# Kernel tuning notes

Measured on AMD Instinct MI355X. Metric: run time of the kernel, lower is better.

The kernel has to match this reference:

```python
import jax, jax.numpy as jnp
import numpy as np

N_NODES = 100000
N_EDGES = 1600000
IN_CH = 128
HID = 128
OUT_CH = 10


def setup_inputs() -> dict:
    key = jax.random.key(0)
    ks = jax.random.split(key, 14)
    s_in = 1.0 / np.sqrt(IN_CH)
    s_h = 1.0 / np.sqrt(HID)
    return {
        "x0": jax.random.normal(ks[0], (N_NODES, IN_CH), jnp.float32),
        "edge_index": jax.random.randint(ks[1], (2, N_EDGES), 0, N_NODES, jnp.int32),
        "edge_weight": jax.random.uniform(ks[2], (N_EDGES,), jnp.float32),
        # GraphConv layer 1 (in -> hid): lin_rel (weight+bias) applied to aggregated msgs, lin_root (no bias)
        "W1_rel": jax.random.uniform(ks[3], (IN_CH, HID), jnp.float32, -s_in, s_in),
        "b1": jax.random.uniform(ks[4], (HID,), jnp.float32, -s_in, s_in),
        "W1_root": jax.random.uniform(ks[5], (IN_CH, HID), jnp.float32, -s_in, s_in),
        # GraphConv layer 2 (hid -> hid)
        "W2_rel": jax.random.uniform(ks[6], (HID, HID), jnp.float32, -s_h, s_h),
        "b2": jax.random.uniform(ks[7], (HID,), jnp.float32, -s_h, s_h),
        "W2_root": jax.random.uniform(ks[8], (HID, HID), jnp.float32, -s_h, s_h),
        # GraphConv layer 3 (hid -> hid)
        "W3_rel": jax.random.uniform(ks[9], (HID, HID), jnp.float32, -s_h, s_h),
        "b3": jax.random.uniform(ks[10], (HID,), jnp.float32, -s_h, s_h),
        "W3_root": jax.random.uniform(ks[11], (HID, HID), jnp.float32, -s_h, s_h),
        # classification head
        "W_lin": jax.random.uniform(ks[12], (HID, OUT_CH), jnp.float32, -s_h, s_h),
        "b_lin": jax.random.uniform(ks[13], (OUT_CH,), jnp.float32, -s_h, s_h),
    }


def _graph_conv(x, src, dst, ew, W_rel, b_rel, W_root):
    # message: x_j * w_e ; aggregate: scatter-add onto dst ; update: lin_rel(agg) + lin_root(x)
    msg = x[src] * ew[:, None]                                   # [E, C]
    agg = jax.ops.segment_sum(msg, dst, num_segments=x.shape[0])  # [N, C]
    return agg @ W_rel + b_rel + x @ W_root                      # [N, C']


def reference(x0, edge_index, edge_weight,
              W1_rel, b1, W1_root,
              W2_rel, b2, W2_root,
              W3_rel, b3, W3_root,
              W_lin, b_lin):
    src, dst = edge_index[0], edge_index[1]
    # dropout p=0.2 is identity in eval mode
    x1 = jax.nn.relu(_graph_conv(x0, src, dst, edge_weight, W1_rel, b1, W1_root))
    x2 = jax.nn.relu(_graph_conv(x1, src, dst, edge_weight, W2_rel, b2, W2_root))
    x3 = jax.nn.relu(_graph_conv(x2, src, dst, edge_weight, W3_rel, b3, W3_root))
    logits = x3 @ W_lin + b_lin
    return jax.nn.log_softmax(logits, axis=-1)
```

## Files before the change

### kernel.cpp

```cpp
#include <hip/hip_runtime.h>
#include <hip/hip_bf16.h>
#include <math.h>

#define C128 128
#define OUT_CH 10

typedef __attribute__((ext_vector_type(8))) short short8;
typedef __attribute__((ext_vector_type(4))) float f32x4;
typedef __attribute__((ext_vector_type(2))) float f32x2;
typedef __attribute__((ext_vector_type(4))) int i32x4;

__device__ __forceinline__ unsigned short f2bf(float f) {
    unsigned b = __float_as_uint(f);
    unsigned r = (b + 0x7FFF + ((b >> 16) & 1)) >> 16;
    return (unsigned short)r;
}
__device__ __forceinline__ float bf2f(unsigned short u) {
    return __uint_as_float(((unsigned)u) << 16);
}


#define NBMAX 400
#define BCAP  4608
#define P1K   4096

__global__ __launch_bounds__(512) void bin_kernel(
    const int* __restrict__ ei, const float* __restrict__ ew,
    int* __restrict__ gcur, unsigned* __restrict__ bins_rec,
    unsigned char* __restrict__ bins_dst, int E, int nb)
{
    __shared__ int cnt[NBMAX];
    __shared__ int pos[NBMAX];
    __shared__ int gbase[NBMAX];
    __shared__ int s[512];
    __shared__ int totalSh;
    __shared__ uint2 buf[P1K];

    const int t = threadIdx.x;
    const int e0 = blockIdx.x * P1K;

    for (int b = t; b < nb; b += 512) { cnt[b] = 0; pos[b] = 0; }
    __syncthreads();

    unsigned rec[8];
    int dstv[8];
    const int e = e0 + t * 8;
    if (e + 8 <= E) {
        i32x4 d0 = __builtin_nontemporal_load((const i32x4*)(ei + E + e));
        i32x4 d1 = __builtin_nontemporal_load((const i32x4*)(ei + E + e + 4));
        i32x4 s0 = __builtin_nontemporal_load((const i32x4*)(ei + e));
        i32x4 s1 = __builtin_nontemporal_load((const i32x4*)(ei + e + 4));
        f32x4 w0 = __builtin_nontemporal_load((const f32x4*)(ew + e));
        f32x4 w1 = __builtin_nontemporal_load((const f32x4*)(ew + e + 4));
        int dd[8] = {d0.x, d0.y, d0.z, d0.w, d1.x, d1.y, d1.z, d1.w};
        int ss[8] = {s0.x, s0.y, s0.z, s0.w, s1.x, s1.y, s1.z, s1.w};
        float ww[8] = {w0.x, w0.y, w0.z, w0.w, w1.x, w1.y, w1.z, w1.w};
#pragma unroll
        for (int j = 0; j < 8; ++j) {
            unsigned wb = __float_as_uint(ww[j]);
            unsigned r  = ((wb + 0x7FFF + ((wb >> 16) & 1)) >> 16) & 0x7FFFu;
            rec[j]  = (unsigned)ss[j] | (r << 17);
            dstv[j] = dd[j];
            atomicAdd(&cnt[dd[j] >> 8], 1);
        }
    } else {
#pragma unroll
        for (int j = 0; j < 8; ++j) {
            int ee = e + j;
            if (ee < E) {
                int dst = ei[E + ee];
                unsigned wb = __float_as_uint(ew[ee]);
                unsigned r  = ((wb + 0x7FFF + ((wb >> 16) & 1)) >> 16) & 0x7FFFu;
                rec[j]  = (unsigned)ei[ee] | (r << 17);
                dstv[j] = dst;
                atomicAdd(&cnt[dst >> 8], 1);
            } else {
                dstv[j] = -1;
            }
        }
    }
    __syncthreads();

    int c = (t < nb) ? cnt[t] : 0;
    s[t] = c;
    __syncthreads();
    for (int o = 1; o < 512; o <<= 1) {
        int u = (t >= o) ? s[t - o] : 0;
        __syncthreads();
        s[t] += u;
        __syncthreads();
    }
    if (t == nb - 1) totalSh = s[t];
    __syncthreads();

#pragma unroll
    for (int j = 0; j < 8; ++j) {
        if (dstv[j] >= 0) {
            int b = dstv[j] >> 8;
            int r = atomicAdd(&pos[b], 1);
            buf[s[b] - cnt[b] + r] = make_uint2(rec[j], (unsigned)dstv[j]);
        }
    }
    __syncthreads();

    if (t < nb) {
        int b = t + (int)((blockIdx.x * 131u) % (unsigned)nb);
        if (b >= nb) b -= nb;
        int cb = cnt[b];
        if (cb > 0) gbase[b] = atomicAdd(&gcur[b], cb);
    }
    __syncthreads();

    const int total = totalSh;
    for (int i = t; i < total; i += 512) {
        uint2 v = buf[i];
        int b = (int)(v.y >> 8);
        int dest = gbase[b] + (i - (s[b] - cnt[b]));
        if (dest < BCAP) {
            bins_rec[(size_t)b * BCAP + dest] = v.x;
            bins_dst[(size_t)b * BCAP + dest] = (unsigned char)(v.y & 255u);
        }
    }
}

__global__ __launch_bounds__(512) void bucket_scan_kernel(
    const int* __restrict__ gcur, int* __restrict__ bbase,
    int* __restrict__ row_ptr, int nb, int N, int E)
{
    __shared__ int s[512];
    int t = threadIdx.x;
    int v = (t < nb) ? gcur[t] : 0;
    s[t] = v;
    __syncthreads();
    for (int o = 1; o < 512; o <<= 1) {
        int u = (t >= o) ? s[t - o] : 0;
        __syncthreads();
        s[t] += u;
        __syncthreads();
    }
    if (t < nb) bbase[t] = s[t] - v;
    if (t == 0) row_ptr[N] = E;
}

__global__ __launch_bounds__(256) void build_kernel(
    const unsigned* __restrict__ bins_rec, const unsigned char* __restrict__ bins_dst,
    const int* __restrict__ gcur, const int* __restrict__ bbase,
    int* __restrict__ row_ptr, unsigned* __restrict__ csr, int N)
{
    __shared__ int rowCnt[256];
    __shared__ int rowOff[256];
    __shared__ int sc[256];
    __shared__ unsigned out[BCAP];

    const int b = blockIdx.x, t = threadIdx.x;
    int cnt = gcur[b];
    if (cnt > BCAP) cnt = BCAP;
    const int base = bbase[b];
    const unsigned* mbr = bins_rec + (size_t)b * BCAP;
    const unsigned char* mbd = bins_dst + (size_t)b * BCAP;

    rowCnt[t] = 0;
    __syncthreads();
    for (int i = t; i < cnt; i += 256) atomicAdd(&rowCnt[(int)mbd[i]], 1);
    __syncthreads();

    int v = rowCnt[t];
    sc[t] = v;
    __syncthreads();
    for (int o = 1; o < 256; o <<= 1) {
        int u = (t >= o) ? sc[t - o] : 0;
        __syncthreads();
        sc[t] += u;
        __syncthreads();
    }
    rowOff[t] = sc[t] - v;
    int idx = b * 256 + t;
    if (idx <= N) row_ptr[idx] = base + sc[t] - v;
    rowCnt[t] = 0;
    __syncthreads();

    for (int i = t; i < cnt; i += 256) {
        int d = (int)mbd[i];
        int k = atomicAdd(&rowCnt[d], 1);
        out[rowOff[d] + k] = mbr[i];
    }
    __syncthreads();

    for (int i = t; i < cnt; i += 256) csr[base + i] = out[i];
}


__global__ __launch_bounds__(256) void cvt_both_kernel(const float4* __restrict__ x,
                                                       ushort4* __restrict__ xb,
                                                       unsigned* __restrict__ xf8, int n4) {
    int i = blockIdx.x * blockDim.x + threadIdx.x;
    if (i < n4) {
        float4 v = x[i];
        ushort4 o;
        o.x = f2bf(v.x); o.y = f2bf(v.y); o.z = f2bf(v.z); o.w = f2bf(v.w);
        xb[i] = o;
        unsigned p = __builtin_amdgcn_cvt_pk_fp8_f32(v.x, v.y, 0, false);
        p = __builtin_amdgcn_cvt_pk_fp8_f32(v.z, v.w, p, true);
        xf8[i] = p;
    }
}


__global__ __launch_bounds__(256) void pack_all_kernel(
    const float* __restrict__ W1r, const float* __restrict__ W1t,
    const float* __restrict__ W2r, const float* __restrict__ W2t,
    const float* __restrict__ W3r, const float* __restrict__ W3t,
    const float* __restrict__ Wl,
    unsigned short* __restrict__ Wp1, unsigned short* __restrict__ Wp2,
    unsigned short* __restrict__ Wp3, unsigned short* __restrict__ WlP)
{
    int b = blockIdx.x;
    if (b < 384) {
        int which = b >> 7;
        const float* Wr = (which == 0) ? W1r : (which == 1) ? W2r : W3r;
        const float* Wt = (which == 0) ? W1t : (which == 1) ? W2t : W3t;
        unsigned short* Wp = (which == 0) ? Wp1 : (which == 1) ? Wp2 : Wp3;
        int idx = (b & 127) * 256 + threadIdx.x;
        int j    = idx & 7;
        int n    = (idx >> 3) & 127;
        int quad = (idx >> 10) & 3;
        int ks   = idx >> 12;
        const float* W = (ks < 4) ? Wr : Wt;
        int k = (ks & 3) * 32 + quad * 8 + j;
        Wp[idx] = f2bf(W[(size_t)k * C128 + n]);
    } else {
        int idx = (b - 384) * 256 + threadIdx.x;
        int j    = idx & 7;
        int col  = (idx >> 3) & 15;
        int quad = (idx >> 7) & 3;
        int ks   = (idx >> 9) & 3;
        int half = idx >> 11;
        int k = ks * 32 + quad * 8 + j;
        float v = (col < OUT_CH) ? Wl[(size_t)k * OUT_CH + col] : 0.f;
        unsigned short hi = f2bf(v);
        unsigned short outv = hi;
        if (half) outv = f2bf(v - bf2f(hi));
        WlP[idx] = outv;
    }
}


__global__ __launch_bounds__(256) void gather_fp8_kernel(
    const unsigned* __restrict__ xf8,
    const int* __restrict__ row_ptr,
    const unsigned* __restrict__ csr, unsigned short* __restrict__ aggb, int N)
{
    int node = blockIdx.x * 4 + (threadIdx.x >> 6);
    if (node >= N) return;
    int lane = threadIdx.x & 63;
    int g   = lane >> 4;
    int l16 = lane & 15;
    int i0  = row_ptr[node];
    int deg = row_ptr[node + 1] - i0;

    f32x2 acc2[4];
#pragma unroll
    for (int j = 0; j < 4; ++j) acc2[j] = (f32x2){0.f, 0.f};

    for (int base = 0; base < deg; base += 64) {
        int rem = deg - base; if (rem > 64) rem = 64;
        int rec = 0;
        if (base + lane < deg)
            rec = (int)__builtin_nontemporal_load(&csr[i0 + base + lane]);

        for (int c = 0; c < rem; c += 16) {
            int i0e = c + g, i1e = c + 4 + g, i2e = c + 8 + g, i3e = c + 12 + g;
            int s0 = __shfl(rec, i0e & 63, 64);
            int s1 = __shfl(rec, i1e & 63, 64);
            int s2 = __shfl(rec, i2e & 63, 64);
            int s3 = __shfl(rec, i3e & 63, 64);
            float w0 = (i0e < rem) ? __uint_as_float(((unsigned)s0 >> 17) << 16) : 0.f;
            float w1 = (i1e < rem) ? __uint_as_float(((unsigned)s1 >> 17) << 16) : 0.f;
            float w2 = (i2e < rem) ? __uint_as_float(((unsigned)s2 >> 17) << 16) : 0.f;
            float w3 = (i3e < rem) ? __uint_as_float(((unsigned)s3 >> 17) << 16) : 0.f;
            uint2 q0 = *(const uint2*)&xf8[(unsigned)(s0 & 0x1FFFF) * 32u + l16 * 2];
            uint2 q1 = *(const uint2*)&xf8[(unsigned)(s1 & 0x1FFFF) * 32u + l16 * 2];
            uint2 q2 = *(const uint2*)&xf8[(unsigned)(s2 & 0x1FFFF) * 32u + l16 * 2];
            uint2 q3 = *(const uint2*)&xf8[(unsigned)(s3 & 0x1FFFF) * 32u + l16 * 2];
#define ACCUM(q, wv)                                                         \
            {                                                                \
                f32x2 w2v = {(wv), (wv)};                                    \
                acc2[0] += __builtin_amdgcn_cvt_pk_f32_fp8((q).x, false) * w2v; \
                acc2[1] += __builtin_amdgcn_cvt_pk_f32_fp8((q).x, true)  * w2v; \
                acc2[2] += __builtin_amdgcn_cvt_pk_f32_fp8((q).y, false) * w2v; \
                acc2[3] += __builtin_amdgcn_cvt_pk_f32_fp8((q).y, true)  * w2v; \
            }
            ACCUM(q0, w0) ACCUM(q1, w1) ACCUM(q2, w2) ACCUM(q3, w3)
#undef ACCUM
        }
    }

#pragma unroll
    for (int j = 0; j < 4; ++j) {
        acc2[j].x += __shfl_xor(acc2[j].x, 16, 64);
        acc2[j].y += __shfl_xor(acc2[j].y, 16, 64);
        acc2[j].x += __shfl_xor(acc2[j].x, 32, 64);
        acc2[j].y += __shfl_xor(acc2[j].y, 32, 64);
    }
    if (g == 0) {
        uint4 o;
        o.x = (unsigned)f2bf(acc2[0].x) | ((unsigned)f2bf(acc2[0].y) << 16);
        o.y = (unsigned)f2bf(acc2[1].x) | ((unsigned)f2bf(acc2[1].y) << 16);
        o.z = (unsigned)f2bf(acc2[2].x) | ((unsigned)f2bf(acc2[2].y) << 16);
        o.w = (unsigned)f2bf(acc2[3].x) | ((unsigned)f2bf(acc2[3].y) << 16);
        *(uint4*)&aggb[(size_t)node * C128 + l16 * 8] = o;
    }
}


__global__ __launch_bounds__(256) void gemm_slim(
    const unsigned short* __restrict__ aggb, const unsigned short* __restrict__ xb,
    const unsigned short* __restrict__ Wp, const float* __restrict__ bias,
    unsigned short* __restrict__ outb, unsigned char* __restrict__ outf8, int N)
{
    const int t = threadIdx.x;
    const int w    = t >> 6;
    const int lane = t & 63;
    const int l15  = lane & 15;
    const int quad = lane >> 4;
    const int wnode0 = blockIdx.x * 64 + w * 16;

    int arow = wnode0 + l15;
    if (arow >= N) arow = N - 1;

    short8 a[8];
#pragma unroll
    for (int k = 0; k < 4; ++k)
        a[k] = *(const short8*)&aggb[(size_t)arow * C128 + k * 32 + quad * 8];
#pragma unroll
    for (int k = 0; k < 4; ++k)
        a[4 + k] = *(const short8*)&xb[(size_t)arow * C128 + k * 32 + quad * 8];

    float bv[8];
#pragma unroll
    for (int nt = 0; nt < 8; ++nt) bv[nt] = bias[nt * 16 + l15];

    f32x4 acc[8];
#pragma unroll
    for (int nt = 0; nt < 8; ++nt) acc[nt] = (f32x4){0.f, 0.f, 0.f, 0.f};

#pragma unroll
    for (int ks = 0; ks < 8; ++ks) {
#pragma unroll
        for (int nt = 0; nt < 8; ++nt) {
            short8 b = *(const short8*)&Wp[(((ks * 4 + quad) * 128) + nt * 16 + l15) * 8];
            acc[nt] = __builtin_amdgcn_mfma_f32_16x16x32_bf16(a[ks], b, acc[nt], 0, 0, 0);
        }
    }

#pragma unroll
    for (int r = 0; r < 4; ++r) {
        int row = wnode0 + quad * 4 + r;
        if (row < N) {
#pragma unroll
            for (int nt = 0; nt < 8; ++nt) {
                float v = fmaxf(acc[nt][r] + bv[nt], 0.f);
                outb[(size_t)row * C128 + nt * 16 + l15] = f2bf(v);
                unsigned p8 = __builtin_amdgcn_cvt_pk_fp8_f32(v, 0.f, 0, false);
                outf8[(size_t)row * C128 + nt * 16 + l15] = (unsigned char)(p8 & 0xff);
            }
        }
    }
}


__global__ __launch_bounds__(256) void gemm_head(
    const unsigned short* __restrict__ aggb, const unsigned short* __restrict__ xb,
    const unsigned short* __restrict__ Wp, const float* __restrict__ bias,
    const unsigned short* __restrict__ WlP, const float* __restrict__ bl,
    float* __restrict__ out, int N)
{
    __shared__ unsigned short X3[4][16 * C128];

    const int t = threadIdx.x;
    const int w    = t >> 6;
    const int lane = t & 63;
    const int l15  = lane & 15;
    const int quad = lane >> 4;
    const int wnode0 = blockIdx.x * 64 + w * 16;

    int arow = wnode0 + l15;
    if (arow >= N) arow = N - 1;

    short8 a[8];
#pragma unroll
    for (int k = 0; k < 4; ++k)
        a[k] = *(const short8*)&aggb[(size_t)arow * C128 + k * 32 + quad * 8];
#pragma unroll
    for (int k = 0; k < 4; ++k)
        a[4 + k] = *(const short8*)&xb[(size_t)arow * C128 + k * 32 + quad * 8];

    float bv[8];
#pragma unroll
    for (int nt = 0; nt < 8; ++nt) bv[nt] = bias[nt * 16 + l15];

    f32x4 acc[8];
#pragma unroll
    for (int nt = 0; nt < 8; ++nt) acc[nt] = (f32x4){0.f, 0.f, 0.f, 0.f};

#pragma unroll
    for (int ks = 0; ks < 8; ++ks) {
#pragma unroll
        for (int nt = 0; nt < 8; ++nt) {
            short8 b = *(const short8*)&Wp[(((ks * 4 + quad) * 128) + nt * 16 + l15) * 8];
            acc[nt] = __builtin_amdgcn_mfma_f32_16x16x32_bf16(a[ks], b, acc[nt], 0, 0, 0);
        }
    }

#pragma unroll
    for (int r = 0; r < 4; ++r) {
        int lrow = quad * 4 + r;
#pragma unroll
        for (int nt = 0; nt < 8; ++nt) {
            float v = fmaxf(acc[nt][r] + bv[nt], 0.f);
            X3[w][lrow * C128 + nt * 16 + l15] = f2bf(v);
        }
    }

    f32x4 hacc = (f32x4){0.f, 0.f, 0.f, 0.f};
#pragma unroll
    for (int ks = 0; ks < 4; ++ks) {
        short8 a2 = *(const short8*)&X3[w][l15 * C128 + ks * 32 + quad * 8];
        short8 bh = *(const short8*)&WlP[(((ks * 4 + quad) * 16) + l15) * 8];
        short8 bl2 = *(const short8*)&WlP[2048 + (((ks * 4 + quad) * 16) + l15) * 8];
        hacc = __builtin_amdgcn_mfma_f32_16x16x32_bf16(a2, bh, hacc, 0, 0, 0);
        hacc = __builtin_amdgcn_mfma_f32_16x16x32_bf16(a2, bl2, hacc, 0, 0, 0);
    }

    float blv = (l15 < OUT_CH) ? bl[l15] : 0.f;
#pragma unroll
    for (int r = 0; r < 4; ++r) {
        int row = wnode0 + quad * 4 + r;
        float lg = (l15 < OUT_CH) ? (hacc[r] + blv) : -1e30f;
        float m = lg;
        m = fmaxf(m, __shfl_xor(m, 1, 64));
        m = fmaxf(m, __shfl_xor(m, 2, 64));
        m = fmaxf(m, __shfl_xor(m, 4, 64));
        m = fmaxf(m, __shfl_xor(m, 8, 64));
        float s = __expf(lg - m);
        s += __shfl_xor(s, 1, 64);
        s += __shfl_xor(s, 2, 64);
        s += __shfl_xor(s, 4, 64);
        s += __shfl_xor(s, 8, 64);
        float lse = m + __logf(s);
        if (l15 < OUT_CH && row < N)
            out[(size_t)row * OUT_CH + l15] = lg - lse;
    }
}


extern "C" void kernel_launch(void* const* d_in, const int* in_sizes, int n_in,
                              void* d_out, int out_size, void* d_ws, size_t ws_size,
                              hipStream_t stream) {
    const float* x0   = (const float*)d_in[0];
    const int*   ei   = (const int*)  d_in[1];
    const float* ew   = (const float*)d_in[2];
    const float* W1r  = (const float*)d_in[3];
    const float* b1   = (const float*)d_in[4];
    const float* W1t  = (const float*)d_in[5];
    const float* W2r  = (const float*)d_in[6];
    const float* b2   = (const float*)d_in[7];
    const float* W2t  = (const float*)d_in[8];
    const float* W3r  = (const float*)d_in[9];
    const float* b3   = (const float*)d_in[10];
    const float* W3t  = (const float*)d_in[11];
    const float* Wlin = (const float*)d_in[12];
    const float* blin = (const float*)d_in[13];

    const int N = in_sizes[0] / C128;
    const int E = in_sizes[1] / 2;
    const int nb = (N + 255) >> 8;

    char* ws = (char*)d_ws;
    size_t off = 0;
    auto alloc = [&](size_t bytes) {
        void* p = ws + off;
        off = (off + bytes + 255) & ~(size_t)255;
        return p;
    };
    size_t bb = (size_t)N * C128 * sizeof(unsigned short);
    size_t fb = (size_t)N * C128;
    unsigned short* aggb = (unsigned short*)alloc(bb);
    unsigned short* xb0  = (unsigned short*)alloc(bb);
    unsigned short* xb1  = (unsigned short*)alloc(bb);
    unsigned char*  xf8  = (unsigned char*)alloc(fb);
    unsigned short* Wp1  = (unsigned short*)alloc(32768 * 2);
    unsigned short* Wp2  = (unsigned short*)alloc(32768 * 2);
    unsigned short* Wp3  = (unsigned short*)alloc(32768 * 2);
    unsigned short* WlP  = (unsigned short*)alloc(4096 * 2);
    unsigned* csr  = (unsigned*)alloc((size_t)E * 4);
    int* row_ptr   = (int*)alloc((size_t)(N + 2) * 4);
    unsigned* bins_rec  = (unsigned*)alloc((size_t)nb * BCAP * 4);
    unsigned char* bins_dst = (unsigned char*)alloc((size_t)nb * BCAP);
    int* gcur      = (int*)alloc((size_t)nb * 4);
    int* bbase     = (int*)alloc((size_t)nb * 4);

    hipMemsetAsync(gcur, 0, (size_t)nb * sizeof(int), stream);
    bin_kernel<<<(E + P1K - 1) / P1K, 512, 0, stream>>>(ei, ew, gcur, bins_rec, bins_dst, E, nb);
    bucket_scan_kernel<<<1, 512, 0, stream>>>(gcur, bbase, row_ptr, nb, N, E);
    build_kernel<<<nb, 256, 0, stream>>>(bins_rec, bins_dst, gcur, bbase, row_ptr, csr, N);

    cvt_both_kernel<<<(N * C128 / 4 + 255) / 256, 256, 0, stream>>>(
        (const float4*)x0, (ushort4*)xb0, (unsigned*)xf8, N * C128 / 4);
    pack_all_kernel<<<400, 256, 0, stream>>>(W1r, W1t, W2r, W2t, W3r, W3t, Wlin,
                                             Wp1, Wp2, Wp3, WlP);

    int gatherGrid = (N + 3) / 4;
    int gemmGrid   = (N + 63) / 64;

    gather_fp8_kernel<<<gatherGrid, 256, 0, stream>>>(
        (const unsigned*)xf8, row_ptr, csr, aggb, N);
    gemm_slim<<<gemmGrid, 256, 0, stream>>>(aggb, xb0, Wp1, b1, xb1, xf8, N);
    gather_fp8_kernel<<<gatherGrid, 256, 0, stream>>>(
        (const unsigned*)xf8, row_ptr, csr, aggb, N);
    gemm_slim<<<gemmGrid, 256, 0, stream>>>(aggb, xb1, Wp2, b2, xb0, xf8, N);
    gather_fp8_kernel<<<gatherGrid, 256, 0, stream>>>(
        (const unsigned*)xf8, row_ptr, csr, aggb, N);
    gemm_head<<<gemmGrid, 256, 0, stream>>>(aggb, xb0, Wp3, b3, WlP, blin,
                                            (float*)d_out, N);
}
```

Measured before the change: 374.7 us.

## Fuse neighbor gather with per-layer GEMM via shared-memory tiles

```diff
diff --git a/kernel.cpp b/kernel.cpp
--- a/kernel.cpp
+++ b/kernel.cpp
@@ -245,211 +245,274 @@
 }
 
 
-__global__ __launch_bounds__(256) void gather_fp8_kernel(
+#define AGS 136
+
+__global__ __launch_bounds__(256) void fused_layer(
     const unsigned* __restrict__ xf8,
     const int* __restrict__ row_ptr,
-    const unsigned* __restrict__ csr, unsigned short* __restrict__ aggb, int N)
-{
-    int node = blockIdx.x * 4 + (threadIdx.x >> 6);
-    if (node >= N) return;
-    int lane = threadIdx.x & 63;
-    int g   = lane >> 4;
-    int l16 = lane & 15;
-    int i0  = row_ptr[node];
-    int deg = row_ptr[node + 1] - i0;
-
-    f32x2 acc2[4];
-#pragma unroll
-    for (int j = 0; j < 4; ++j) acc2[j] = (f32x2){0.f, 0.f};
-
-    for (int base = 0; base < deg; base += 64) {
-        int rem = deg - base; if (rem > 64) rem = 64;
-        int rec = 0;
-        if (base + lane < deg)
-            rec = (int)__builtin_nontemporal_load(&csr[i0 + base + lane]);
-
-        for (int c = 0; c < rem; c += 16) {
-            int i0e = c + g, i1e = c + 4 + g, i2e = c + 8 + g, i3e = c + 12 + g;
-            int s0 = __shfl(rec, i0e & 63, 64);
-            int s1 = __shfl(rec, i1e & 63, 64);
-            int s2 = __shfl(rec, i2e & 63, 64);
-            int s3 = __shfl(rec, i3e & 63, 64);
-            float w0 = (i0e < rem) ? __uint_as_float(((unsigned)s0 >> 17) << 16) : 0.f;
-            float w1 = (i1e < rem) ? __uint_as_float(((unsigned)s1 >> 17) << 16) : 0.f;
-            float w2 = (i2e < rem) ? __uint_as_float(((unsigned)s2 >> 17) << 16) : 0.f;
-            float w3 = (i3e < rem) ? __uint_as_float(((unsigned)s3 >> 17) << 16) : 0.f;
-            uint2 q0 = *(const uint2*)&xf8[(unsigned)(s0 & 0x1FFFF) * 32u + l16 * 2];
-            uint2 q1 = *(const uint2*)&xf8[(unsigned)(s1 & 0x1FFFF) * 32u + l16 * 2];
-            uint2 q2 = *(const uint2*)&xf8[(unsigned)(s2 & 0x1FFFF) * 32u + l16 * 2];
-            uint2 q3 = *(const uint2*)&xf8[(unsigned)(s3 & 0x1FFFF) * 32u + l16 * 2];
-#define ACCUM(q, wv)                                                         \
-            {                                                                \
-                f32x2 w2v = {(wv), (wv)};                                    \
-                acc2[0] += __builtin_amdgcn_cvt_pk_f32_fp8((q).x, false) * w2v; \
-                acc2[1] += __builtin_amdgcn_cvt_pk_f32_fp8((q).x, true)  * w2v; \
-                acc2[2] += __builtin_amdgcn_cvt_pk_f32_fp8((q).y, false) * w2v; \
-                acc2[3] += __builtin_amdgcn_cvt_pk_f32_fp8((q).y, true)  * w2v; \
-            }
-            ACCUM(q0, w0) ACCUM(q1, w1) ACCUM(q2, w2) ACCUM(q3, w3)
-#undef ACCUM
-        }
-    }
-
-#pragma unroll
-    for (int j = 0; j < 4; ++j) {
-        acc2[j].x += __shfl_xor(acc2[j].x, 16, 64);
-        acc2[j].y += __shfl_xor(acc2[j].y, 16, 64);
-        acc2[j].x += __shfl_xor(acc2[j].x, 32, 64);
-        acc2[j].y += __shfl_xor(acc2[j].y, 32, 64);
-    }
-    if (g == 0) {
-        uint4 o;
-        o.x = (unsigned)f2bf(acc2[0].x) | ((unsigned)f2bf(acc2[0].y) << 16);
-        o.y = (unsigned)f2bf(acc2[1].x) | ((unsigned)f2bf(acc2[1].y) << 16);
-        o.z = (unsigned)f2bf(acc2[2].x) | ((unsigned)f2bf(acc2[2].y) << 16);
-        o.w = (unsigned)f2bf(acc2[3].x) | ((unsigned)f2bf(acc2[3].y) << 16);
-        *(uint4*)&aggb[(size_t)node * C128 + l16 * 8] = o;
-    }
-}
-
-
-__global__ __launch_bounds__(256) void gemm_slim(
-    const unsigned short* __restrict__ aggb, const unsigned short* __restrict__ xb,
-    const unsigned short* __restrict__ Wp, const float* __restrict__ bias,
+    const unsigned* __restrict__ csr,
+    const unsigned short* __restrict__ xb,
+    const unsigned short* __restrict__ Wp,
+    const float* __restrict__ bias,
     unsigned short* __restrict__ outb, unsigned char* __restrict__ outf8, int N)
 {
+    __shared__ unsigned short AG[16 * AGS];
+    __shared__ unsigned short XR[16 * AGS];
+
     const int t = threadIdx.x;
     const int w    = t >> 6;
     const int lane = t & 63;
-    const int l15  = lane & 15;
-    const int quad = lane >> 4;
-    const int wnode0 = blockIdx.x * 64 + w * 16;
-
-    int arow = wnode0 + l15;
-    if (arow >= N) arow = N - 1;
-
-    short8 a[8];
-#pragma unroll
-    for (int k = 0; k < 4; ++k)
-        a[k] = *(const short8*)&aggb[(size_t)arow * C128 + k * 32 + quad * 8];
-#pragma unroll
-    for (int k = 0; k < 4; ++k)
-        a[4 + k] = *(const short8*)&xb[(size_t)arow * C128 + k * 32 + quad * 8];
-
-    float bv[8];
-#pragma unroll
-    for (int nt = 0; nt < 8; ++nt) bv[nt] = bias[nt * 16 + l15];
-
-    f32x4 acc[8];
-#pragma unroll
-    for (int nt = 0; nt < 8; ++nt) acc[nt] = (f32x4){0.f, 0.f, 0.f, 0.f};
+    const int l16  = lane & 15;
+    const int g    = lane >> 4;
+    const int tile0 = blockIdx.x * 16;
+
+    {
+        int rrow = tile0 + w * 4 + g;
+        int srow = (rrow < N) ? rrow : 0;
+        uint4 v = *(const uint4*)&xb[(size_t)srow * C128 + l16 * 8];
+        *(uint4*)&XR[(w * 4 + g) * AGS + l16 * 8] = v;
+    }
+
+    for (int i = 0; i < 4; ++i) {
+        int node = tile0 + w * 4 + i;
+        int i0 = 0, deg = 0;
+        if (node < N) { i0 = row_ptr[node]; deg = row_ptr[node + 1] - i0; }
+
+        f32x2 acc2[4];
+#pragma unroll
+        for (int j = 0; j < 4; ++j) acc2[j] = (f32x2){0.f, 0.f};
+
+        for (int base = 0; base < deg; base += 64) {
+            int rem = deg - base; if (rem > 64) rem = 64;
+            int rec = 0;
+            if (base + lane < deg)
+                rec = (int)__builtin_nontemporal_load(&csr[i0 + base + lane]);
+
+            for (int c = 0; c < rem; c += 16) {
+                int i0e = c + g, i1e = c + 4 + g, i2e = c + 8 + g, i3e = c + 12 + g;
+                int s0 = __shfl(rec, i0e & 63, 64);
+                int s1 = __shfl(rec, i1e & 63, 64);
+                int s2 = __shfl(rec, i2e & 63, 64);
+                int s3 = __shfl(rec, i3e & 63, 64);
+                float w0 = (i0e < rem) ? __uint_as_float(((unsigned)s0 >> 17) << 16) : 0.f;
+                float w1 = (i1e < rem) ? __uint_as_float(((unsigned)s1 >> 17) << 16) : 0.f;
+                float w2 = (i2e < rem) ? __uint_as_float(((unsigned)s2 >> 17) << 16) : 0.f;
+                float w3 = (i3e < rem) ? __uint_as_float(((unsigned)s3 >> 17) << 16) : 0.f;
+                uint2 q0 = *(const uint2*)&xf8[(unsigned)(s0 & 0x1FFFF) * 32u + l16 * 2];
+                uint2 q1 = *(const uint2*)&xf8[(unsigned)(s1 & 0x1FFFF) * 32u + l16 * 2];
+                uint2 q2 = *(const uint2*)&xf8[(unsigned)(s2 & 0x1FFFF) * 32u + l16 * 2];
+                uint2 q3 = *(const uint2*)&xf8[(unsigned)(s3 & 0x1FFFF) * 32u + l16 * 2];
+#define ACCUM(q, wv)                                                         \
+                {                                                            \
+                    f32x2 w2v = {(wv), (wv)};                                \
+                    acc2[0] += __builtin_amdgcn_cvt_pk_f32_fp8((q).x, false) * w2v; \
+                    acc2[1] += __builtin_amdgcn_cvt_pk_f32_fp8((q).x, true)  * w2v; \
+                    acc2[2] += __builtin_amdgcn_cvt_pk_f32_fp8((q).y, false) * w2v; \
+                    acc2[3] += __builtin_amdgcn_cvt_pk_f32_fp8((q).y, true)  * w2v; \
+                }
+                ACCUM(q0, w0) ACCUM(q1, w1) ACCUM(q2, w2) ACCUM(q3, w3)
+#undef ACCUM
+            }
+        }
+
+#pragma unroll
+        for (int j = 0; j < 4; ++j) {
+            acc2[j].x += __shfl_xor(acc2[j].x, 16, 64);
+            acc2[j].y += __shfl_xor(acc2[j].y, 16, 64);
+            acc2[j].x += __shfl_xor(acc2[j].x, 32, 64);
+            acc2[j].y += __shfl_xor(acc2[j].y, 32, 64);
+        }
+        if (g == 0) {
+            uint4 o;
+            o.x = (unsigned)f2bf(acc2[0].x) | ((unsigned)f2bf(acc2[0].y) << 16);
+            o.y = (unsigned)f2bf(acc2[1].x) | ((unsigned)f2bf(acc2[1].y) << 16);
+            o.z = (unsigned)f2bf(acc2[2].x) | ((unsigned)f2bf(acc2[2].y) << 16);
+            o.w = (unsigned)f2bf(acc2[3].x) | ((unsigned)f2bf(acc2[3].y) << 16);
+            *(uint4*)&AG[(w * 4 + i) * AGS + l16 * 8] = o;
+        }
+    }
+    __syncthreads();
+
+    const int l15 = l16, quad = g;
+    const int nt0 = 2 * w, nt1 = 2 * w + 1;
+    float bv0 = bias[nt0 * 16 + l15];
+    float bv1 = bias[nt1 * 16 + l15];
+    f32x4 acc0 = (f32x4){0.f, 0.f, 0.f, 0.f};
+    f32x4 acc1 = (f32x4){0.f, 0.f, 0.f, 0.f};
 
 #pragma unroll
     for (int ks = 0; ks < 8; ++ks) {
-#pragma unroll
-        for (int nt = 0; nt < 8; ++nt) {
-            short8 b = *(const short8*)&Wp[(((ks * 4 + quad) * 128) + nt * 16 + l15) * 8];
-            acc[nt] = __builtin_amdgcn_mfma_f32_16x16x32_bf16(a[ks], b, acc[nt], 0, 0, 0);
-        }
+        short8 a;
+        if (ks < 4) a = *(const short8*)&AG[l15 * AGS + ks * 32 + quad * 8];
+        else        a = *(const short8*)&XR[l15 * AGS + (ks - 4) * 32 + quad * 8];
+        short8 b0 = *(const short8*)&Wp[(((ks * 4 + quad) * 128) + nt0 * 16 + l15) * 8];
+        short8 b1 = *(const short8*)&Wp[(((ks * 4 + quad) * 128) + nt1 * 16 + l15) * 8];
+        acc0 = __builtin_amdgcn_mfma_f32_16x16x32_bf16(a, b0, acc0, 0, 0, 0);
+        acc1 = __builtin_amdgcn_mfma_f32_16x16x32_bf16(a, b1, acc1, 0, 0, 0);
     }
 
 #pragma unroll
     for (int r = 0; r < 4; ++r) {
-        int row = wnode0 + quad * 4 + r;
+        int row = tile0 + quad * 4 + r;
         if (row < N) {
-#pragma unroll
-            for (int nt = 0; nt < 8; ++nt) {
-                float v = fmaxf(acc[nt][r] + bv[nt], 0.f);
-                outb[(size_t)row * C128 + nt * 16 + l15] = f2bf(v);
-                unsigned p8 = __builtin_amdgcn_cvt_pk_fp8_f32(v, 0.f, 0, false);
-                outf8[(size_t)row * C128 + nt * 16 + l15] = (unsigned char)(p8 & 0xff);
-            }
-        }
-    }
-}
-
-
-__global__ __launch_bounds__(256) void gemm_head(
-    const unsigned short* __restrict__ aggb, const unsigned short* __restrict__ xb,
-    const unsigned short* __restrict__ Wp, const float* __restrict__ bias,
+            float v0 = fmaxf(acc0[r] + bv0, 0.f);
+            float v1 = fmaxf(acc1[r] + bv1, 0.f);
+            outb[(size_t)row * C128 + nt0 * 16 + l15] = f2bf(v0);
+            outb[(size_t)row * C128 + nt1 * 16 + l15] = f2bf(v1);
+            unsigned p0 = __builtin_amdgcn_cvt_pk_fp8_f32(v0, 0.f, 0, false);
+            unsigned p1 = __builtin_amdgcn_cvt_pk_fp8_f32(v1, 0.f, 0, false);
+            outf8[(size_t)row * C128 + nt0 * 16 + l15] = (unsigned char)(p0 & 0xff);
+            outf8[(size_t)row * C128 + nt1 * 16 + l15] = (unsigned char)(p1 & 0xff);
+        }
+    }
+}
+
+
+__global__ __launch_bounds__(256) void fused_layer_head(
+    const unsigned* __restrict__ xf8,
+    const int* __restrict__ row_ptr,
+    const unsigned* __restrict__ csr,
+    const unsigned short* __restrict__ xb,
+    const unsigned short* __restrict__ Wp,
+    const float* __restrict__ bias,
     const unsigned short* __restrict__ WlP, const float* __restrict__ bl,
     float* __restrict__ out, int N)
 {
-    __shared__ unsigned short X3[4][16 * C128];
+    __shared__ unsigned short AG[16 * AGS];
+    __shared__ unsigned short XR[16 * AGS];
 
     const int t = threadIdx.x;
     const int w    = t >> 6;
     const int lane = t & 63;
-    const int l15  = lane & 15;
-    const int quad = lane >> 4;
-    const int wnode0 = blockIdx.x * 64 + w * 16;
-
-    int arow = wnode0 + l15;
-    if (arow >= N) arow = N - 1;
-
-    short8 a[8];
-#pragma unroll
-    for (int k = 0; k < 4; ++k)
-        a[k] = *(const short8*)&aggb[(size_t)arow * C128 + k * 32 + quad * 8];
-#pragma unroll
-    for (int k = 0; k < 4; ++k)
-        a[4 + k] = *(const short8*)&xb[(size_t)arow * C128 + k * 32 + quad * 8];
-
-    float bv[8];
-#pragma unroll
-    for (int nt = 0; nt < 8; ++nt) bv[nt] = bias[nt * 16 + l15];
-
-    f32x4 acc[8];
-#pragma unroll
-    for (int nt = 0; nt < 8; ++nt) acc[nt] = (f32x4){0.f, 0.f, 0.f, 0.f};
+    const int l16  = lane & 15;
+    const int g    = lane >> 4;
+    const int tile0 = blockIdx.x * 16;
+
+    {
+        int rrow = tile0 + w * 4 + g;
+        int srow = (rrow < N) ? rrow : 0;
+        uint4 v = *(const uint4*)&xb[(size_t)srow * C128 + l16 * 8];
+        *(uint4*)&XR[(w * 4 + g) * AGS + l16 * 8] = v;
+    }
+
+    for (int i = 0; i < 4; ++i) {
+        int node = tile0 + w * 4 + i;
+        int i0 = 0, deg = 0;
+        if (node < N) { i0 = row_ptr[node]; deg = row_ptr[node + 1] - i0; }
+
+        f32x2 acc2[4];
+#pragma unroll
+        for (int j = 0; j < 4; ++j) acc2[j] = (f32x2){0.f, 0.f};
+
+        for (int base = 0; base < deg; base += 64) {
+            int rem = deg - base; if (rem > 64) rem = 64;
+            int rec = 0;
+            if (base + lane < deg)
+                rec = (int)__builtin_nontemporal_load(&csr[i0 + base + lane]);
+
+            for (int c = 0; c < rem; c += 16) {
+                int i0e = c + g, i1e = c + 4 + g, i2e = c + 8 + g, i3e = c + 12 + g;
+                int s0 = __shfl(rec, i0e & 63, 64);
+                int s1 = __shfl(rec, i1e & 63, 64);
+                int s2 = __shfl(rec, i2e & 63, 64);
+                int s3 = __shfl(rec, i3e & 63, 64);
+                float w0 = (i0e < rem) ? __uint_as_float(((unsigned)s0 >> 17) << 16) : 0.f;
+                float w1 = (i1e < rem) ? __uint_as_float(((unsigned)s1 >> 17) << 16) : 0.f;
+                float w2 = (i2e < rem) ? __uint_as_float(((unsigned)s2 >> 17) << 16) : 0.f;
+                float w3 = (i3e < rem) ? __uint_as_float(((unsigned)s3 >> 17) << 16) : 0.f;
+                uint2 q0 = *(const uint2*)&xf8[(unsigned)(s0 & 0x1FFFF) * 32u + l16 * 2];
+                uint2 q1 = *(const uint2*)&xf8[(unsigned)(s1 & 0x1FFFF) * 32u + l16 * 2];
+                uint2 q2 = *(const uint2*)&xf8[(unsigned)(s2 & 0x1FFFF) * 32u + l16 * 2];
+                uint2 q3 = *(const uint2*)&xf8[(unsigned)(s3 & 0x1FFFF) * 32u + l16 * 2];
+#define ACCUM(q, wv)                                                         \
+                {                                                            \
+                    f32x2 w2v = {(wv), (wv)};                                \
+                    acc2[0] += __builtin_amdgcn_cvt_pk_f32_fp8((q).x, false) * w2v; \
+                    acc2[1] += __builtin_amdgcn_cvt_pk_f32_fp8((q).x, true)  * w2v; \
+                    acc2[2] += __builtin_amdgcn_cvt_pk_f32_fp8((q).y, false) * w2v; \
+                    acc2[3] += __builtin_amdgcn_cvt_pk_f32_fp8((q).y, true)  * w2v; \
+                }
+                ACCUM(q0, w0) ACCUM(q1, w1) ACCUM(q2, w2) ACCUM(q3, w3)
+#undef ACCUM
+            }
+        }
+
+#pragma unroll
+        for (int j = 0; j < 4; ++j) {
+            acc2[j].x += __shfl_xor(acc2[j].x, 16, 64);
+            acc2[j].y += __shfl_xor(acc2[j].y, 16, 64);
+            acc2[j].x += __shfl_xor(acc2[j].x, 32, 64);
+            acc2[j].y += __shfl_xor(acc2[j].y, 32, 64);
+        }
+        if (g == 0) {
+            uint4 o;
+            o.x = (unsigned)f2bf(acc2[0].x) | ((unsigned)f2bf(acc2[0].y) << 16);
+            o.y = (unsigned)f2bf(acc2[1].x) | ((unsigned)f2bf(acc2[1].y) << 16);
+            o.z = (unsigned)f2bf(acc2[2].x) | ((unsigned)f2bf(acc2[2].y) << 16);
+            o.w = (unsigned)f2bf(acc2[3].x) | ((unsigned)f2bf(acc2[3].y) << 16);
+            *(uint4*)&AG[(w * 4 + i) * AGS + l16 * 8] = o;
+        }
+    }
+    __syncthreads();
+
+    const int l15 = l16, quad = g;
+    const int nt0 = 2 * w, nt1 = 2 * w + 1;
+    float bv0 = bias[nt0 * 16 + l15];
+    float bv1 = bias[nt1 * 16 + l15];
+    f32x4 acc0 = (f32x4){0.f, 0.f, 0.f, 0.f};
+    f32x4 acc1 = (f32x4){0.f, 0.f, 0.f, 0.f};
 
 #pragma unroll
     for (int ks = 0; ks < 8; ++ks) {
-#pragma unroll
-        for (int nt = 0; nt < 8; ++nt) {
-            short8 b = *(const short8*)&Wp[(((ks * 4 + quad) * 128) + nt * 16 + l15) * 8];
-            acc[nt] = __builtin_amdgcn_mfma_f32_16x16x32_bf16(a[ks], b, acc[nt], 0, 0, 0);
-        }
-    }
-
+        short8 a;
+        if (ks < 4) a = *(const short8*)&AG[l15 * AGS + ks * 32 + quad * 8];
+        else        a = *(const short8*)&XR[l15 * AGS + (ks - 4) * 32 + quad * 8];
+        short8 b0 = *(const short8*)&Wp[(((ks * 4 + quad) * 128) + nt0 * 16 + l15) * 8];
+        short8 b1 = *(const short8*)&Wp[(((ks * 4 + quad) * 128) + nt1 * 16 + l15) * 8];
+        acc0 = __builtin_amdgcn_mfma_f32_16x16x32_bf16(a, b0, acc0, 0, 0, 0);
+        acc1 = __builtin_amdgcn_mfma_f32_16x16x32_bf16(a, b1, acc1, 0, 0, 0);
+    }
+
+    __syncthreads();
 #pragma unroll
     for (int r = 0; r < 4; ++r) {
         int lrow = quad * 4 + r;
-#pragma unroll
-        for (int nt = 0; nt < 8; ++nt) {
-            float v = fmaxf(acc[nt][r] + bv[nt], 0.f);
-            X3[w][lrow * C128 + nt * 16 + l15] = f2bf(v);
-        }
-    }
-
-    f32x4 hacc = (f32x4){0.f, 0.f, 0.f, 0.f};
-#pragma unroll
-    for (int ks = 0; ks < 4; ++ks) {
-        short8 a2 = *(const short8*)&X3[w][l15 * C128 + ks * 32 + quad * 8];
-        short8 bh = *(const short8*)&WlP[(((ks * 4 + quad) * 16) + l15) * 8];
-        short8 bl2 = *(const short8*)&WlP[2048 + (((ks * 4 + quad) * 16) + l15) * 8];
-        hacc = __builtin_amdgcn_mfma_f32_16x16x32_bf16(a2, bh, hacc, 0, 0, 0);
-        hacc = __builtin_amdgcn_mfma_f32_16x16x32_bf16(a2, bl2, hacc, 0, 0, 0);
-    }
-
-    float blv = (l15 < OUT_CH) ? bl[l15] : 0.f;
-#pragma unroll
-    for (int r = 0; r < 4; ++r) {
-        int row = wnode0 + quad * 4 + r;
-        float lg = (l15 < OUT_CH) ? (hacc[r] + blv) : -1e30f;
-        float m = lg;
-        m = fmaxf(m, __shfl_xor(m, 1, 64));
-        m = fmaxf(m, __shfl_xor(m, 2, 64));
-        m = fmaxf(m, __shfl_xor(m, 4, 64));
-        m = fmaxf(m, __shfl_xor(m, 8, 64));
-        float s = __expf(lg - m);
-        s += __shfl_xor(s, 1, 64);
-        s += __shfl_xor(s, 2, 64);
-        s += __shfl_xor(s, 4, 64);
-        s += __shfl_xor(s, 8, 64);
-        float lse = m + __logf(s);
-        if (l15 < OUT_CH && row < N)
-            out[(size_t)row * OUT_CH + l15] = lg - lse;
+        float v0 = fmaxf(acc0[r] + bv0, 0.f);
+        float v1 = fmaxf(acc1[r] + bv1, 0.f);
+        AG[lrow * AGS + nt0 * 16 + l15] = f2bf(v0);
+        AG[lrow * AGS + nt1 * 16 + l15] = f2bf(v1);
+    }
+    __syncthreads();
+
+    if (w == 0) {
+        f32x4 hacc = (f32x4){0.f, 0.f, 0.f, 0.f};
+#pragma unroll
+        for (int ks = 0; ks < 4; ++ks) {
+            short8 a2  = *(const short8*)&AG[l15 * AGS + ks * 32 + quad * 8];
+            short8 bh  = *(const short8*)&WlP[(((ks * 4 + quad) * 16) + l15) * 8];
+            short8 bl2 = *(const short8*)&WlP[2048 + (((ks * 4 + quad) * 16) + l15) * 8];
+            hacc = __builtin_amdgcn_mfma_f32_16x16x32_bf16(a2, bh, hacc, 0, 0, 0);
+            hacc = __builtin_amdgcn_mfma_f32_16x16x32_bf16(a2, bl2, hacc, 0, 0, 0);
+        }
+        float blv = (l15 < OUT_CH) ? bl[l15] : 0.f;
+#pragma unroll
+        for (int r = 0; r < 4; ++r) {
+            int row = tile0 + quad * 4 + r;
+            float lg = (l15 < OUT_CH) ? (hacc[r] + blv) : -1e30f;
+            float m = lg;
+            m = fmaxf(m, __shfl_xor(m, 1, 64));
+            m = fmaxf(m, __shfl_xor(m, 2, 64));
+            m = fmaxf(m, __shfl_xor(m, 4, 64));
+            m = fmaxf(m, __shfl_xor(m, 8, 64));
+            float s = __expf(lg - m);
+            s += __shfl_xor(s, 1, 64);
+            s += __shfl_xor(s, 2, 64);
+            s += __shfl_xor(s, 4, 64);
+            s += __shfl_xor(s, 8, 64);
+            float lse = m + __logf(s);
+            if (l15 < OUT_CH && row < N)
+                out[(size_t)row * OUT_CH + l15] = lg - lse;
+        }
     }
 }
 
@@ -485,10 +548,10 @@
     };
     size_t bb = (size_t)N * C128 * sizeof(unsigned short);
     size_t fb = (size_t)N * C128;
-    unsigned short* aggb = (unsigned short*)alloc(bb);
     unsigned short* xb0  = (unsigned short*)alloc(bb);
     unsigned short* xb1  = (unsigned short*)alloc(bb);
-    unsigned char*  xf8  = (unsigned char*)alloc(fb);
+    unsigned char*  xf8a = (unsigned char*)alloc(fb);
+    unsigned char*  xf8b = (unsigned char*)alloc(fb);
     unsigned short* Wp1  = (unsigned short*)alloc(32768 * 2);
     unsigned short* Wp2  = (unsigned short*)alloc(32768 * 2);
     unsigned short* Wp3  = (unsigned short*)alloc(32768 * 2);
@@ -506,21 +569,17 @@
     build_kernel<<<nb, 256, 0, stream>>>(bins_rec, bins_dst, gcur, bbase, row_ptr, csr, N);
 
     cvt_both_kernel<<<(N * C128 / 4 + 255) / 256, 256, 0, stream>>>(
-        (const float4*)x0, (ushort4*)xb0, (unsigned*)xf8, N * C128 / 4);
+        (const float4*)x0, (ushort4*)xb0, (unsigned*)xf8a, N * C128 / 4);
     pack_all_kernel<<<400, 256, 0, stream>>>(W1r, W1t, W2r, W2t, W3r, W3t, Wlin,
                                              Wp1, Wp2, Wp3, WlP);
 
-    int gatherGrid = (N + 3) / 4;
-    int gemmGrid   = (N + 63) / 64;
-
-    gather_fp8_kernel<<<gatherGrid, 256, 0, stream>>>(
-        (const unsigned*)xf8, row_ptr, csr, aggb, N);
-    gemm_slim<<<gemmGrid, 256, 0, stream>>>(aggb, xb0, Wp1, b1, xb1, xf8, N);
-    gather_fp8_kernel<<<gatherGrid, 256, 0, stream>>>(
-        (const unsigned*)xf8, row_ptr, csr, aggb, N);
-    gemm_slim<<<gemmGrid, 256, 0, stream>>>(aggb, xb1, Wp2, b2, xb0, xf8, N);
-    gather_fp8_kernel<<<gatherGrid, 256, 0, stream>>>(
-        (const unsigned*)xf8, row_ptr, csr, aggb, N);
-    gemm_head<<<gemmGrid, 256, 0, stream>>>(aggb, xb0, Wp3, b3, WlP, blin,
-                                            (float*)d_out, N);
-}
+    const int fusedGrid = (N + 15) / 16;
+
+    fused_layer<<<fusedGrid, 256, 0, stream>>>(
+        (const unsigned*)xf8a, row_ptr, csr, xb0, Wp1, b1, xb1, xf8b, N);
+    fused_layer<<<fusedGrid, 256, 0, stream>>>(
+        (const unsigned*)xf8b, row_ptr, csr, xb1, Wp2, b2, xb0, xf8a, N);
+    fused_layer_head<<<fusedGrid, 256, 0, stream>>>(
+        (const unsigned*)xf8a, row_ptr, csr, xb0, Wp3, b3, WlP, blin,
+        (float*)d_out, N);
+}
```

Result: faster. 366.3 us (-2.3%).
